# Optimization experiments

Hardware: AMD Instinct MI355X
Metric: run time of the kernel (lower is better)

## Reference

```python
import jax, jax.numpy as jnp
import numpy as np

B, S, D = 4, 2048, 1024


def setup_inputs() -> dict:
    key = jax.random.key(0)
    ks = jax.random.split(key, 7)
    scale = 1.0 / np.sqrt(D)  # mimic torch Linear default init scale
    x = jax.random.normal(ks[0], (B, S, D), dtype=jnp.float32)
    Wq = jax.random.uniform(ks[1], (D, D), jnp.float32, -scale, scale)
    bq = jax.random.uniform(ks[2], (D,), jnp.float32, -scale, scale)
    Wk = jax.random.uniform(ks[3], (D, D), jnp.float32, -scale, scale)
    bk = jax.random.uniform(ks[4], (D,), jnp.float32, -scale, scale)
    Wv = jax.random.uniform(ks[5], (D, D), jnp.float32, -scale, scale)
    bv = jax.random.uniform(ks[6], (D,), jnp.float32, -scale, scale)
    return {"x": x, "Wq": Wq, "bq": bq, "Wk": Wk, "bk": bk, "Wv": Wv, "bv": bv}


def reference(x, Wq, bq, Wk, bk, Wv, bv):
    # Linear projections (torch Linear: x @ W.T + b; here W stored as [in, out])
    q = jnp.einsum("bsd,de->bse", x, Wq) + bq
    k = jnp.einsum("bsd,de->bse", x, Wk) + bk
    v = jnp.einsum("bsd,de->bse", x, Wv) + bv
    # NOTE: original module applies NO 1/sqrt(d) scaling — faithful to source.
    scores = jnp.einsum("bqd,bkd->bqk", q, k)  # [B, S, S]
    attn = jax.nn.softmax(scores, axis=-1)
    return jnp.einsum("bqk,bkd->bqd", attn, v)
```

## Files before the change

kernel.cpp:

```cpp
#include <hip/hip_runtime.h>
#include <stdint.h>

typedef unsigned short ushort_t;
typedef _Float16 f16;
typedef __attribute__((ext_vector_type(8))) _Float16 half8;
typedef __attribute__((ext_vector_type(4))) _Float16 half4;
typedef __attribute__((ext_vector_type(4))) float float4v;

#define AS1 __attribute__((address_space(1)))
#define AS3 __attribute__((address_space(3)))

static __device__ __forceinline__ void gload16(const void* g, void* l) {
    __builtin_amdgcn_global_load_lds((const AS1 unsigned int*)g,
                                     (AS3 unsigned int*)l, 16, 0, 0);
}

template<int IM, int OUT, bool BIAS>
__global__ __launch_bounds__(256, IM == 8 ? 2 : 4)
void gemm_k(const f16* __restrict__ A, const f16* __restrict__ B,
            const float* __restrict__ bias,
            float* __restrict__ Cf, f16* __restrict__ Ch, f16* __restrict__ Vt,
            int K, int lda, int ldb, int ldc,
            long zsA, long zsB, long zsC)
{
    constexpr int R = IM * 32;
    extern __shared__ f16 smem[];
    f16* sA0 = smem;
    f16* sA1 = smem + R * 32;
    f16* sB0 = smem + 2 * R * 32;
    f16* sB1 = sB0 + 4096;

    const long zb = blockIdx.z;
    A += zb * zsA; B += zb * zsB;

    const int t  = threadIdx.x;
    const int bm = blockIdx.x * R;
    const int bn = blockIdx.y * 128;

    const int  srow = t >> 2;
    const int  skg  = (t & 3) * 8;
    const f16* gA = A + (long)(bm + srow) * lda + skg;
    const f16* gB = B + (long)(bn + srow) * ldb + skg;
    const long rstepA = (long)64 * lda;
    const long rstepB = (long)64 * ldb;

    const int lane = t & 63;
    const int wv   = t >> 6;
    const int wm   = (wv & 1) * (IM * 16);
    const int wn   = (wv >> 1) * 64;
    const int lm   = lane & 15;
    const int q    = lane >> 4;

    float4v acc[IM][4];
    #pragma unroll
    for (int i = 0; i < IM; ++i)
        #pragma unroll
        for (int j = 0; j < 4; ++j)
            #pragma unroll
            for (int r = 0; r < 4; ++r) acc[i][j][r] = 0.f;

    for (int kt = 0; kt < K; kt += 64) {
        __syncthreads();
        #pragma unroll
        for (int r = 0; r < R / 64; ++r) {
            gload16(gA + kt      + r * rstepA, sA0 + r * 2048 + t * 8);
            gload16(gA + kt + 32 + r * rstepA, sA1 + r * 2048 + t * 8);
        }
        #pragma unroll
        for (int r = 0; r < 2; ++r) {
            gload16(gB + kt      + r * rstepB, sB0 + r * 2048 + t * 8);
            gload16(gB + kt + 32 + r * rstepB, sB1 + r * 2048 + t * 8);
        }
        __syncthreads();

        #pragma unroll
        for (int ks = 0; ks < 2; ++ks) {
            const f16* sA = ks ? sA1 : sA0;
            const f16* sB = ks ? sB1 : sB0;
            half8 a[IM], b[4];
            #pragma unroll
            for (int i = 0; i < IM; ++i)
                a[i] = *(const half8*)(sA + (wm + i * 16 + lm) * 32 + q * 8);
            #pragma unroll
            for (int j = 0; j < 4; ++j)
                b[j] = *(const half8*)(sB + (wn + j * 16 + lm) * 32 + q * 8);
            #pragma unroll
            for (int i = 0; i < IM; ++i)
                #pragma unroll
                for (int j = 0; j < 4; ++j)
                    acc[i][j] = __builtin_amdgcn_mfma_f32_16x16x32_f16(a[i], b[j], acc[i][j], 0, 0, 0);
        }
    }

    #pragma unroll
    for (int i = 0; i < IM; ++i) {
        const int rowb = bm + wm + i * 16 + q * 4;
        #pragma unroll
        for (int j = 0; j < 4; ++j) {
            const int col = bn + wn + j * 16 + lm;
            const float bv_ = BIAS ? bias[col] : 0.f;
            if (OUT == 4 && col >= 2048) {
                half4 pk;
                #pragma unroll
                for (int r = 0; r < 4; ++r) pk[r] = (f16)(acc[i][j][r] + bv_);
                *(half4*)(Vt + ((long)(rowb >> 11) * 1024 + (col - 2048)) * 2048 + (rowb & 2047)) = pk;
            } else {
                #pragma unroll
                for (int r = 0; r < 4; ++r) {
                    const float val = acc[i][j][r] + bv_;
                    const int row = rowb + r;
                    if (OUT == 0)      Cf[zb * zsC + (long)row * ldc + col] = val;
                    else if (OUT == 1) Ch[zb * zsC + (long)row * ldc + col] = (f16)val;
                    else               Ch[(long)row * ldc + col] = (f16)val;
                }
            }
        }
    }
}

__global__ __launch_bounds__(256)
void preproc_k(const float* __restrict__ x,
               const float* __restrict__ Wq, const float* __restrict__ Wk,
               const float* __restrict__ Wv,
               const float* __restrict__ bq, const float* __restrict__ bk,
               const float* __restrict__ bv,
               f16* __restrict__ xh, f16* __restrict__ WT, float* __restrict__ bqkv)
{
    __shared__ float tile[64][65];
    const int bx = blockIdx.x;
    const int t  = threadIdx.x;

    if (bx < 8192) {
        const long i = ((long)bx * 256 + t) * 4;
        const float4v v = *(const float4v*)(x + i);
        half4 h;
        #pragma unroll
        for (int j = 0; j < 4; ++j) h[j] = (f16)v[j];
        *(half4*)(xh + i) = h;
    } else if (bx < 8960) {
        const int f = bx - 8192;
        const int z = f >> 8;
        const int rem = f & 255;
        const int n0 = (rem & 15) * 64;
        const int k0 = (rem >> 4) * 64;
        const float* W = (z == 0) ? Wq : (z == 1) ? Wk : Wv;
        f16* T = WT + (long)z * 1048576;
        #pragma unroll
        for (int i = 0; i < 4; ++i) {
            const int r = (t >> 4) + i * 16;
            const int c = (t & 15) * 4;
            const float4v v = *(const float4v*)(W + (long)(k0 + r) * 1024 + n0 + c);
            tile[r][c + 0] = v[0]; tile[r][c + 1] = v[1];
            tile[r][c + 2] = v[2]; tile[r][c + 3] = v[3];
        }
        __syncthreads();
        #pragma unroll
        for (int i = 0; i < 4; ++i) {
            const int nr = (t >> 4) + i * 16;
            const int c  = (t & 15) * 4;
            half4 h;
            #pragma unroll
            for (int j = 0; j < 4; ++j) h[j] = (f16)tile[c + j][nr];
            *(half4*)(T + (long)(n0 + nr) * 1024 + k0 + c) = h;
        }
    } else {
        const int i = (bx - 8960) * 256 + t;
        bqkv[i] = (i < 1024) ? bq[i] : (i < 2048) ? bk[i - 1024] : bv[i - 2048];
    }
}

__global__ __launch_bounds__(256)
void softmax_k(f16* __restrict__ Sc)
{
    const int t = threadIdx.x;
    const long row = blockIdx.x;
    half8* p = (half8*)(Sc + row * 2048);
    const half8 hv = p[t];
    float xv[8];
    #pragma unroll
    for (int j = 0; j < 8; ++j) xv[j] = (float)hv[j];

    float m = -1e30f;
    #pragma unroll
    for (int j = 0; j < 8; ++j) m = fmaxf(m, xv[j]);
    #pragma unroll
    for (int off = 32; off; off >>= 1) m = fmaxf(m, __shfl_xor(m, off, 64));
    __shared__ float r1[4], r2[4];
    if ((t & 63) == 0) r1[t >> 6] = m;
    __syncthreads();
    m = fmaxf(fmaxf(r1[0], r1[1]), fmaxf(r1[2], r1[3]));

    float s = 0.f;
    #pragma unroll
    for (int j = 0; j < 8; ++j) { xv[j] = __expf(xv[j] - m); s += xv[j]; }
    #pragma unroll
    for (int off = 32; off; off >>= 1) s += __shfl_xor(s, off, 64);
    if ((t & 63) == 0) r2[t >> 6] = s;
    __syncthreads();
    s = r2[0] + r2[1] + r2[2] + r2[3];
    const float inv = 1.f / s;

    half8 o;
    #pragma unroll
    for (int j = 0; j < 8; ++j) o[j] = (f16)(xv[j] * inv);
    p[t] = o;
}

extern "C" void kernel_launch(void* const* d_in, const int* in_sizes, int n_in,
                              void* d_out, int out_size, void* d_ws, size_t ws_size,
                              hipStream_t stream)
{
    const float* x  = (const float*)d_in[0];
    const float* Wq = (const float*)d_in[1];
    const float* bq = (const float*)d_in[2];
    const float* Wk = (const float*)d_in[3];
    const float* bk = (const float*)d_in[4];
    const float* Wv = (const float*)d_in[5];
    const float* bv = (const float*)d_in[6];
    float* out = (float*)d_out;

    char* ws = (char*)d_ws;
    const long MiB = 1024 * 1024;
    f16*   xh   = (f16*)  (ws + 0);
    f16*   WT   = (f16*)  (ws + 16 * MiB);
    float* bqkv = (float*)(ws + 22 * MiB);
    f16*   scores = (f16*) (ws + 0);
    f16*   qk     = (f16*) (ws + 64 * MiB);
    f16*   vT     = (f16*) (ws + 96 * MiB);

    preproc_k<<<8972, 256, 0, stream>>>(x, Wq, Wk, Wv, bq, bk, bv, xh, WT, bqkv);

    gemm_k<8, 4, true><<<dim3(32, 24, 1), 256, 49152, stream>>>(
        xh, WT, bqkv, nullptr, qk, vT,
        1024, 1024, 1024, 2048, 0, 0, 0);

    const long SS = (long)2048 * 2048;
    gemm_k<8, 1, false><<<dim3(8, 16, 4), 256, 49152, stream>>>(
        qk, qk + 1024, nullptr, nullptr, scores, nullptr,
        1024, 2048, 2048, 2048, SS, SS, SS);
    softmax_k<<<8192, 256, 0, stream>>>(scores);
    gemm_k<4, 0, false><<<dim3(16, 8, 4), 256, 32768, stream>>>(
        scores, vT, nullptr, out, nullptr, nullptr,
        2048, 2048, 2048, 1024, SS, (long)1024 * 2048, (long)2048 * 1024);
}
```

Before: 264.1 us.

## Double-buffer GEMM K-loop with prefetch of next stage and partial vmcnt waits

The GEMM main loop now works in 32-wide K stages and issues the global-to-LDS loads for stage s+1 before computing stage s. It waits with an explicit vmcnt that leaves only the newest stage's loads outstanding. The goal is to overlap global-load latency with MFMA work, where before the loop stalled on every load batch. The two LDS halves become ping-pong buffers guarded by scheduler-fenced barriers, so there are now two barriers per 32-element step instead of per 64, which adds synchronisation overhead.

```diff
diff --git a/kernel.cpp b/kernel.cpp
--- a/kernel.cpp
+++ b/kernel.cpp
@@ -13,6 +13,12 @@
 static __device__ __forceinline__ void gload16(const void* g, void* l) {
     __builtin_amdgcn_global_load_lds((const AS1 unsigned int*)g,
                                      (AS3 unsigned int*)l, 16, 0, 0);
+}
+
+static __device__ __forceinline__ void barrier_nodrain() {
+    __builtin_amdgcn_sched_barrier(0);
+    __builtin_amdgcn_s_barrier();
+    __builtin_amdgcn_sched_barrier(0);
 }
 
 template<int IM, int OUT, bool BIAS>
@@ -23,12 +29,10 @@
             int K, int lda, int ldb, int ldc,
             long zsA, long zsB, long zsC)
 {
-    constexpr int R = IM * 32;
+    constexpr int R    = IM * 32;
+    constexpr int AH   = R * 32;
+    constexpr int NLD  = R / 64 + 2;
     extern __shared__ f16 smem[];
-    f16* sA0 = smem;
-    f16* sA1 = smem + R * 32;
-    f16* sB0 = smem + 2 * R * 32;
-    f16* sB1 = sB0 + 4096;
 
     const long zb = blockIdx.z;
     A += zb * zsA; B += zb * zsB;
@@ -59,37 +63,47 @@
             #pragma unroll
             for (int r = 0; r < 4; ++r) acc[i][j][r] = 0.f;
 
-    for (int kt = 0; kt < K; kt += 64) {
-        __syncthreads();
-        #pragma unroll
-        for (int r = 0; r < R / 64; ++r) {
-            gload16(gA + kt      + r * rstepA, sA0 + r * 2048 + t * 8);
-            gload16(gA + kt + 32 + r * rstepA, sA1 + r * 2048 + t * 8);
-        }
-        #pragma unroll
-        for (int r = 0; r < 2; ++r) {
-            gload16(gB + kt      + r * rstepB, sB0 + r * 2048 + t * 8);
-            gload16(gB + kt + 32 + r * rstepB, sB1 + r * 2048 + t * 8);
-        }
-        __syncthreads();
-
-        #pragma unroll
-        for (int ks = 0; ks < 2; ++ks) {
-            const f16* sA = ks ? sA1 : sA0;
-            const f16* sB = ks ? sB1 : sB0;
-            half8 a[IM], b[4];
-            #pragma unroll
-            for (int i = 0; i < IM; ++i)
-                a[i] = *(const half8*)(sA + (wm + i * 16 + lm) * 32 + q * 8);
+    auto stage = [&](int s) {
+        const int kk  = s << 5;
+        const int buf = s & 1;
+        f16* dA = smem + buf * AH;
+        f16* dB = smem + 2 * AH + buf * 4096;
+        #pragma unroll
+        for (int r = 0; r < R / 64; ++r)
+            gload16(gA + kk + r * rstepA, dA + r * 2048 + t * 8);
+        #pragma unroll
+        for (int r = 0; r < 2; ++r)
+            gload16(gB + kk + r * rstepB, dB + r * 2048 + t * 8);
+    };
+
+    const int nstage = K >> 5;
+    stage(0);
+    for (int s = 0; s < nstage; ++s) {
+        if (s + 1 < nstage) {
+            stage(s + 1);
+            __builtin_amdgcn_s_waitcnt(0x0F70 | NLD);
+        } else {
+            __builtin_amdgcn_s_waitcnt(0x0F70);
+        }
+        barrier_nodrain();
+
+        const int buf = s & 1;
+        const f16* sA = smem + buf * AH;
+        const f16* sB = smem + 2 * AH + buf * 4096;
+        half8 a[IM], b[4];
+        #pragma unroll
+        for (int i = 0; i < IM; ++i)
+            a[i] = *(const half8*)(sA + (wm + i * 16 + lm) * 32 + q * 8);
+        #pragma unroll
+        for (int j = 0; j < 4; ++j)
+            b[j] = *(const half8*)(sB + (wn + j * 16 + lm) * 32 + q * 8);
+        #pragma unroll
+        for (int i = 0; i < IM; ++i)
             #pragma unroll
             for (int j = 0; j < 4; ++j)
-                b[j] = *(const half8*)(sB + (wn + j * 16 + lm) * 32 + q * 8);
-            #pragma unroll
-            for (int i = 0; i < IM; ++i)
-                #pragma unroll
-                for (int j = 0; j < 4; ++j)
-                    acc[i][j] = __builtin_amdgcn_mfma_f32_16x16x32_f16(a[i], b[j], acc[i][j], 0, 0, 0);
-        }
+                acc[i][j] = __builtin_amdgcn_mfma_f32_16x16x32_f16(a[i], b[j], acc[i][j], 0, 0, 0);
+
+        barrier_nodrain();
     }
 
     #pragma unroll
```

New measurement: 253.1 us. -4.2%, faster.
